# Kernel tuning notes

Measured on AMD Instinct MI355X. Metric: run time of the kernel, lower is better.

## Reference

```python
import jax, jax.numpy as jnp
import numpy as np

N, E, G = 100000, 3200000, 5000
EPS = 1e-5
HEADS, HC = 8, 16


def setup_inputs() -> dict:
    key = jax.random.key(0)
    k = jax.random.split(key, 12)

    def lin(kk, fi, fo):
        return (jax.random.normal(kk, (fi, fo), jnp.float32) / np.sqrt(fi)).astype(jnp.float32)

    return {
        "x": jax.random.normal(k[0], (N, 20), jnp.float32),
        "edge_index": jax.random.randint(k[1], (2, E), 0, N, dtype=jnp.int32),
        "batch": jnp.sort(jax.random.randint(k[2], (N,), 0, G, dtype=jnp.int32)),
        "W1": lin(k[3], 20, 64), "b1": jnp.zeros((64,), jnp.float32),
        "g1": jnp.ones((64,), jnp.float32), "be1": jnp.zeros((64,), jnp.float32),
        "W2": lin(k[4], 64, 32), "b2": jnp.zeros((32,), jnp.float32),
        "g2": jnp.ones((32,), jnp.float32), "be2": jnp.zeros((32,), jnp.float32),
        "W3": lin(k[5], 32, 16), "b3": jnp.zeros((16,), jnp.float32),
        "g3": jnp.ones((16,), jnp.float32), "be3": jnp.zeros((16,), jnp.float32),
        "Wg": lin(k[6], 16, HEADS * HC),
        "att_src": jax.random.normal(k[7], (HEADS, HC), jnp.float32) * 0.1,
        "att_dst": jax.random.normal(k[8], (HEADS, HC), jnp.float32) * 0.1,
        "bg": jnp.zeros((HC,), jnp.float32),
        "Wf": lin(k[9], 16, 3), "bf": jnp.zeros((3,), jnp.float32),
    }


def reference(x, edge_index, batch,
              W1, b1, g1, be1, W2, b2, g2, be2, W3, b3, g3, be3,
              Wg, att_src, att_dst, bg, Wf, bf):
    src, dst = edge_index[0], edge_index[1]
    loop = jnp.arange(N, dtype=src.dtype)
    src_sl = jnp.concatenate([src, loop])  # self-loops (GCN + GAT add_self_loops)
    dst_sl = jnp.concatenate([dst, loop])

    # GCN symmetric normalization D^-1/2 (A+I) D^-1/2
    deg = jax.ops.segment_sum(jnp.ones_like(src_sl, dtype=jnp.float32), dst_sl, N)
    dinv = jnp.where(deg > 0, 1.0 / jnp.sqrt(deg), 0.0)
    norm = (dinv[src_sl] * dinv[dst_sl])[:, None]  # [E+N, 1]

    def gcn(h, W, b):
        h = h @ W
        return jax.ops.segment_sum(h[src_sl] * norm, dst_sl, N) + b

    def bn_relu(h, g, b):  # BatchNorm1d (train-mode batch stats) + ReLU
        mu = h.mean(0)
        var = ((h - mu) ** 2).mean(0)
        return jax.nn.relu(g * (h - mu) * jax.lax.rsqrt(var + EPS) + b)

    h = bn_relu(gcn(x, W1, b1), g1, be1)   # dropout = identity (eval)
    h = bn_relu(gcn(h, W2, b2), g2, be2)
    h = bn_relu(gcn(h, W3, b3), g3, be3)

    # GATConv: heads=8, concat=False (mean over heads), eval -> no dropout
    xg = (h @ Wg).reshape(N, HEADS, HC)
    a_src = (xg * att_src).sum(-1)  # [N, H]
    a_dst = (xg * att_dst).sum(-1)
    logit = jax.nn.leaky_relu(a_src[src_sl] + a_dst[dst_sl], 0.2)  # [E+N, H]
    m = jax.ops.segment_max(logit, dst_sl, N)          # segment softmax over dst
    e = jnp.exp(logit - m[dst_sl])
    s = jax.ops.segment_sum(e, dst_sl, N)
    alpha = e / s[dst_sl]
    agg = jax.ops.segment_sum(xg[src_sl] * alpha[:, :, None], dst_sl, N)  # [N,H,C]
    hg = agg.mean(1) + bg  # [N, 16]

    pooled = jax.ops.segment_sum(hg, batch, G)  # global_add_pool -> [G, 16]
    return pooled @ Wf + bf  # [G, 3]
```

## Files before the change

kernel.cpp:

```cpp
#include <hip/hip_runtime.h>
#include <hip/hip_fp16.h>

constexpr int NN = 100000;
constexpr int EE = 3200000;
constexpr int GG = 5000;
constexpr float BNEPS = 1e-5f;

constexpr int BINS = 128;
constexpr int NPB = (NN + BINS - 1) / BINS;
constexpr int BCHUNK = 8192;
constexpr int NBCH = (EE + BCHUNK - 1) / BCHUNK;
constexpr int BINCAP2 = 96;
constexpr int BINREG = 27648;
constexpr int LCAP = 26624;
constexpr int CTR_STRIDE = 32;

typedef int int4v __attribute__((ext_vector_type(4)));


__global__ __launch_bounds__(1024) void bin_edges(const int* __restrict__ ei,
                                                  uint2* __restrict__ pairs,
                                                  int* __restrict__ binCur) {
    __shared__ int bcnt[BINS];
    __shared__ int bbase[BINS];
    __shared__ uint2 buf[BINS][BINCAP2];
    const int t = threadIdx.x;
    const int lane = t & 63, wv = t >> 6;
    for (int ch = blockIdx.x; ch < NBCH; ch += gridDim.x) {
        for (int k = t; k < BINS; k += 1024) bcnt[k] = 0;
        __syncthreads();
        const int qbase = ch * (BCHUNK / 4);
#pragma unroll
        for (int rep = 0; rep < 2; ++rep) {
            const int q = qbase + rep * 1024 + t;
            if (q < EE / 4) {
                int4v d = __builtin_nontemporal_load((const int4v*)(ei + EE) + q);
                int4v s = __builtin_nontemporal_load((const int4v*)ei + q);
                int dd[4] = {d.x, d.y, d.z, d.w};
                int ss[4] = {s.x, s.y, s.z, s.w};
#pragma unroll
                for (int k = 0; k < 4; ++k) {
                    int o = dd[k] / NPB;
                    int p = atomicAdd(&bcnt[o], 1);
                    if (p < BINCAP2) {
                        buf[o][p] = make_uint2((unsigned)dd[k], (unsigned)ss[k]);
                    } else {
                        int gp = atomicAdd(&binCur[o * CTR_STRIDE], 1);
                        pairs[(size_t)o * BINREG + gp] =
                            make_uint2((unsigned)dd[k], (unsigned)ss[k]);
                    }
                }
            }
        }
        __syncthreads();
        if (t < BINS) {
            int c = bcnt[t] < BINCAP2 ? bcnt[t] : BINCAP2;
            bbase[t] = atomicAdd(&binCur[t * CTR_STRIDE], c);
            bcnt[t] = c;
        }
        __syncthreads();
        for (int o = wv; o < BINS; o += 16) {
            const int c = bcnt[o];
            const size_t base = (size_t)o * BINREG + bbase[o];
            for (int k = lane; k < c; k += 64) pairs[base + k] = buf[o][k];
        }
        __syncthreads();
    }
}


__global__ void bin_base(const int* __restrict__ binCur, int* __restrict__ binBase) {
    __shared__ int s[BINS];
    const int t = threadIdx.x;
    const int v = binCur[t * CTR_STRIDE];
    s[t] = v;
    __syncthreads();
    for (int off = 1; off < BINS; off <<= 1) {
        int add = (t >= off) ? s[t - off] : 0;
        __syncthreads();
        s[t] += add;
        __syncthreads();
    }
    binBase[t] = s[t] - v;
}


__global__ __launch_bounds__(1024) void scatter_lds(const uint2* __restrict__ pairs,
                                                    const int* __restrict__ binCur,
                                                    const int* __restrict__ binBase,
                                                    int* __restrict__ rowptr,
                                                    float* __restrict__ dinv,
                                                    int* __restrict__ colA) {
    __shared__ int scnt[NPB];
    __shared__ int sscan[1024];
    __shared__ int lbuf[LCAP];
    const int b = blockIdx.x;
    const int t = threadIdx.x;
    const int lo = b * NPB;
    const int hi = (lo + NPB < NN) ? lo + NPB : NN;
    const int nb = hi - lo;
    const int tot = binCur[b * CTR_STRIDE];
    const int base = binBase[b];
    const uint2* p = pairs + (size_t)b * BINREG;
    for (int k = t; k < nb; k += 1024) scnt[k] = 0;
    __syncthreads();
    for (int q = t; q < tot; q += 1024) atomicAdd(&scnt[p[q].x - lo], 1);
    __syncthreads();
    const int myc = (t < nb) ? scnt[t] : 0;
    sscan[t] = myc;
    __syncthreads();
    for (int off = 1; off < 1024; off <<= 1) {
        int add = (t >= off) ? sscan[t - off] : 0;
        __syncthreads();
        sscan[t] += add;
        __syncthreads();
    }
    const int excl = sscan[t] - myc;
    if (t < nb) {
        rowptr[lo + t] = base + excl;
        dinv[lo + t] = rsqrtf((float)(myc + 1));
        scnt[t] = excl;
    }
    if (b == BINS - 1 && t == 0) rowptr[NN] = base + tot;
    __syncthreads();
    for (int q = t; q < tot; q += 1024) {
        uint2 e = p[q];
        int pos = atomicAdd(&scnt[e.x - lo], 1);
        if (pos < LCAP) lbuf[pos] = (int)e.y;
        else colA[base + pos] = (int)e.y;
    }
    __syncthreads();
    const int m = tot < LCAP ? tot : LCAP;
    for (int k = t; k < m; k += 1024) colA[base + k] = lbuf[k];
}


__global__ void scale_x(const float* __restrict__ x, const float* __restrict__ dinv,
                        __half* __restrict__ xsc) {
    int idx = blockIdx.x * blockDim.x + threadIdx.x;
    if (idx < NN * 20) {
        int n = idx / 20;
        xsc[idx] = __float2half(x[idx] * dinv[n]);
    }
}


template <int FIN, int FOUT, bool AFFINE, bool SCALED, bool STATS>
__global__ void gemm_k(const float* __restrict__ hin,
                       const float* __restrict__ sumsIn, const float* __restrict__ ssqIn,
                       const float* __restrict__ g, const float* __restrict__ be,
                       const float* __restrict__ W, const float* __restrict__ dinv,
                       const float* __restrict__ bias,
                       float* __restrict__ outF, __half* __restrict__ outH,
                       float* __restrict__ sumsOut, float* __restrict__ ssqOut) {
    constexpr int NB = 256 / FOUT;
    __shared__ float Wl[FIN * FOUT];
    __shared__ float rows[NB][FIN];
    __shared__ float aa[AFFINE ? FIN : 1], bb[AFFINE ? FIN : 1];
    const int t = threadIdx.x;
    if constexpr (AFFINE) {
        if (t < FIN) {
            float mu = sumsIn[t] / (float)NN;
            float var = ssqIn[t] / (float)NN - mu * mu;
            float a = g[t] * rsqrtf(var + BNEPS);
            aa[t] = a;
            bb[t] = be[t] - mu * a;
        }
    }
    for (int i = t; i < FIN * FOUT; i += 256) Wl[i] = W[i];
    const int c = t % FOUT, s = t / FOUT;
    const int ngrp = (NN + NB - 1) / NB;
    float sAcc = 0.f, qAcc = 0.f;
    for (int grp = blockIdx.x; grp < ngrp; grp += gridDim.x) {
        __syncthreads();
        for (int i = t; i < NB * FIN; i += 256) {
            int sn = i / FIN, k = i % FIN;
            int n2 = grp * NB + sn;
            float v = 0.f;
            if (n2 < NN) {
                v = hin[(size_t)n2 * FIN + k];
                if constexpr (AFFINE) {
                    v = aa[k] * v + bb[k];
                    v = v > 0.f ? v : 0.f;
                }
            }
            rows[sn][k] = v;
        }
        __syncthreads();
        int node = grp * NB + s;
        if (node < NN) {
            float acc = 0.f;
#pragma unroll
            for (int k = 0; k < FIN; ++k) acc += rows[s][k] * Wl[k * FOUT + c];
            if constexpr (SCALED) {
                outH[(size_t)node * FOUT + c] = __float2half(acc * dinv[node]);
            } else {
                float val = acc + bias[c];
                outF[(size_t)node * FOUT + c] = val;
                if constexpr (STATS) { sAcc += val; qAcc += val * val; }
            }
        }
    }
    if constexpr (STATS) {
        __shared__ float ls[FOUT], lq[FOUT];
        __syncthreads();
        if (t < FOUT) { ls[t] = 0.f; lq[t] = 0.f; }
        __syncthreads();
        atomicAdd(&ls[c], sAcc);
        atomicAdd(&lq[c], qAcc);
        __syncthreads();
        if (t < FOUT) { atomicAdd(&sumsOut[t], ls[t]); atomicAdd(&ssqOut[t], lq[t]); }
    }
}


template <int H2, int OUTF, bool STATS>
__global__ void agg_half(const __half2* __restrict__ src, const int* __restrict__ rowptr,
                         const int* __restrict__ colA, const float* __restrict__ dinv,
                         const float* __restrict__ bias, float* __restrict__ out,
                         float* __restrict__ sumsOut, float* __restrict__ ssqOut) {
    constexpr int SUB = 64 / H2;
    const int lane = threadIdx.x & 63;
    const int wid = (blockIdx.x * blockDim.x + threadIdx.x) >> 6;
    const int totalWaves = (gridDim.x * blockDim.x) >> 6;
    const int f = lane % H2;
    const int sub = lane / H2;
    const int stride = totalWaves * SUB;
    float bx = 0.f, by = 0.f;
    if (bias != nullptr) {
        bx = bias[2 * f];
        by = (2 * f + 1 < OUTF) ? bias[2 * f + 1] : 0.f;
    }
    const int i0 = (sub < SUB) ? wid * SUB + sub : NN;
    float sx = 0.f, qx = 0.f, sy = 0.f, qy = 0.f;
    for (int i = i0; i < NN; i += stride) {
        const int r0 = rowptr[i], r1 = rowptr[i + 1];
        float2 acc = __half22float2(src[(size_t)i * H2 + f]);
        float2 acc2 = {0.f, 0.f};
        int e = r0;
        for (; e + 3 < r1; e += 4) {
            int j0 = colA[e], j1 = colA[e + 1], j2 = colA[e + 2], j3 = colA[e + 3];
            float2 v0 = __half22float2(src[(size_t)j0 * H2 + f]);
            float2 v1 = __half22float2(src[(size_t)j1 * H2 + f]);
            float2 v2 = __half22float2(src[(size_t)j2 * H2 + f]);
            float2 v3 = __half22float2(src[(size_t)j3 * H2 + f]);
            acc.x += v0.x + v1.x;
            acc.y += v0.y + v1.y;
            acc2.x += v2.x + v3.x;
            acc2.y += v2.y + v3.y;
        }
        for (; e < r1; ++e) {
            float2 v = __half22float2(src[(size_t)colA[e] * H2 + f]);
            acc.x += v.x; acc.y += v.y;
        }
        acc.x += acc2.x; acc.y += acc2.y;
        const float d = dinv[i];
        float vx = d * acc.x + bx;
        out[(size_t)i * OUTF + 2 * f] = vx;
        if constexpr (STATS) { sx += vx; qx += vx * vx; }
        if (2 * f + 1 < OUTF) {
            float vy = d * acc.y + by;
            out[(size_t)i * OUTF + 2 * f + 1] = vy;
            if constexpr (STATS) { sy += vy; qy += vy * vy; }
        }
    }
    if constexpr (STATS) {
        __shared__ float ls[OUTF], lq[OUTF];
        const int t = threadIdx.x;
        if (t < OUTF) { ls[t] = 0.f; lq[t] = 0.f; }
        __syncthreads();
        atomicAdd(&ls[2 * f], sx);
        atomicAdd(&lq[2 * f], qx);
        if (2 * f + 1 < OUTF) {
            atomicAdd(&ls[2 * f + 1], sy);
            atomicAdd(&lq[2 * f + 1], qy);
        }
        __syncthreads();
        if (t < OUTF) { atomicAdd(&sumsOut[t], ls[t]); atomicAdd(&ssqOut[t], lq[t]); }
    }
}


__global__ void gat_mats(const float* __restrict__ Wg, const float* __restrict__ att_src,
                         const float* __restrict__ att_dst, const float* __restrict__ Wf,
                         const float* __restrict__ bg, float* __restrict__ Psrc,
                         float* __restrict__ Pdst, float* __restrict__ M,
                         float* __restrict__ bgW) {
    int t = threadIdx.x;
    if (t < 128) {
        int k = t >> 3, h = t & 7;
        float s = 0.f, d = 0.f;
        for (int c = 0; c < 16; ++c) {
            float wv = Wg[k * 128 + h * 16 + c];
            s += wv * att_src[h * 16 + c];
            d += wv * att_dst[h * 16 + c];
        }
        Psrc[k * 8 + h] = s;
        Pdst[k * 8 + h] = d;
    } else if (t < 512) {
        int m = t - 128;
        if (m < 384) {
            int hk = m / 3, j = m - hk * 3;
            int H = hk >> 4, k = hk & 15;
            float s = 0.f;
            for (int c = 0; c < 16; ++c) s += Wg[k * 128 + H * 16 + c] * Wf[c * 3 + j];
            M[hk * 3 + j] = 0.125f * s;
        }
    } else if (t < 515) {
        int j = t - 512;
        float s = 0.f;
        for (int c = 0; c < 16; ++c) s += bg[c] * Wf[c * 3 + j];
        bgW[j] = s;
    }
}


__global__ void gat_pre2(const float* __restrict__ h3,
                         const float* __restrict__ sums3, const float* __restrict__ ssq3,
                         const float* __restrict__ g3, const float* __restrict__ be3,
                         const float* __restrict__ Psrc, const float* __restrict__ Pdst,
                         __half* __restrict__ z, float* __restrict__ asrc,
                         float* __restrict__ adst) {
    __shared__ float Ps[128], Pd[128], aa[16], bb[16];
    int t = threadIdx.x;
    if (t < 128) { Ps[t] = Psrc[t]; Pd[t] = Pdst[t]; }
    if (t < 16) {
        float mu = sums3[t] / (float)NN;
        float var = ssq3[t] / (float)NN - mu * mu;
        float a = g3[t] * rsqrtf(var + BNEPS);
        aa[t] = a;
        bb[t] = be3[t] - mu * a;
    }
    __syncthreads();
    int n = blockIdx.x * blockDim.x + t;
    if (n >= NN) return;
    float zv[16];
#pragma unroll
    for (int k = 0; k < 16; ++k) {
        float v = h3[(size_t)n * 16 + k];
        v = aa[k] * v + bb[k];
        zv[k] = v > 0.f ? v : 0.f;
    }
    __half2 zh[8];
#pragma unroll
    for (int k = 0; k < 8; ++k) zh[k] = __floats2half2_rn(zv[2 * k], zv[2 * k + 1]);
    float4* zo = (float4*)(z + (size_t)n * 16);
    zo[0] = ((float4*)zh)[0];
    zo[1] = ((float4*)zh)[1];
    float as[8], ad[8];
#pragma unroll
    for (int h = 0; h < 8; ++h) { as[h] = 0.f; ad[h] = 0.f; }
#pragma unroll
    for (int k = 0; k < 16; ++k) {
        float zk = zv[k];
#pragma unroll
        for (int h = 0; h < 8; ++h) {
            as[h] += zk * Ps[k * 8 + h];
            ad[h] += zk * Pd[k * 8 + h];
        }
    }
    float4* a4 = (float4*)(asrc + (size_t)n * 8);
    a4[0] = make_float4(as[0], as[1], as[2], as[3]);
    a4[1] = make_float4(as[4], as[5], as[6], as[7]);
    float4* d4 = (float4*)(adst + (size_t)n * 8);
    d4[0] = make_float4(ad[0], ad[1], ad[2], ad[3]);
    d4[1] = make_float4(ad[4], ad[5], ad[6], ad[7]);
}


__device__ __forceinline__ float leaky02(float x) { return x > 0.f ? x : 0.2f * x; }

__global__ void gat_agg5(const float2* __restrict__ z2, const float* __restrict__ asrc,
                         const float* __restrict__ adst, const int* __restrict__ rowptr,
                         const int* __restrict__ colA, __half* __restrict__ Sn) {
    const int lane = threadIdx.x & 63;
    const int q = lane & 3;
    const int hh = (lane >> 2) & 1;
    const int sub = lane >> 3;
    const int wid = (blockIdx.x * blockDim.x + threadIdx.x) >> 6;
    const int totalWaves = (gridDim.x * blockDim.x) >> 6;
    const float4* asrc4 = (const float4*)asrc;
    const float4* adst4 = (const float4*)adst;
    for (int i = wid; i < NN; i += totalWaves) {
        const int r0 = rowptr[i], r1 = rowptr[i + 1];
        const float4 adh = adst4[(size_t)i * 2 + hh];
        float acc[4][4];
        float wsum[4];
        {
            float4 a = asrc4[(size_t)i * 2 + hh];
            float2 zr = z2[(size_t)i * 4 + q];
            const __half2* zp = (const __half2*)&zr;
            float2 f0 = __half22float2(zp[0]), f1 = __half22float2(zp[1]);
            float zf[4] = {f0.x, f0.y, f1.x, f1.y};
            float wq[4];
            wq[0] = (sub == 0) ? __expf(leaky02(a.x + adh.x)) : 0.f;
            wq[1] = (sub == 0) ? __expf(leaky02(a.y + adh.y)) : 0.f;
            wq[2] = (sub == 0) ? __expf(leaky02(a.z + adh.z)) : 0.f;
            wq[3] = (sub == 0) ? __expf(leaky02(a.w + adh.w)) : 0.f;
#pragma unroll
            for (int h = 0; h < 4; ++h) {
                wsum[h] = wq[h];
#pragma unroll
                for (int k = 0; k < 4; ++k) acc[h][k] = wq[h] * zf[k];
            }
        }
        for (int e = r0; e < r1; e += 8) {
            const int ee = e + sub;
            const bool val = ee < r1;
            const int j = val ? colA[ee] : i;
            float4 a = asrc4[(size_t)j * 2 + hh];
            float2 zr = z2[(size_t)j * 4 + q];
            const __half2* zp = (const __half2*)&zr;
            float2 f0 = __half22float2(zp[0]), f1 = __half22float2(zp[1]);
            float zf[4] = {f0.x, f0.y, f1.x, f1.y};
            float wq[4];
            wq[0] = val ? __expf(leaky02(a.x + adh.x)) : 0.f;
            wq[1] = val ? __expf(leaky02(a.y + adh.y)) : 0.f;
            wq[2] = val ? __expf(leaky02(a.z + adh.z)) : 0.f;
            wq[3] = val ? __expf(leaky02(a.w + adh.w)) : 0.f;
#pragma unroll
            for (int h = 0; h < 4; ++h) {
                wsum[h] += wq[h];
#pragma unroll
                for (int k = 0; k < 4; ++k) acc[h][k] += wq[h] * zf[k];
            }
        }
#pragma unroll
        for (int off = 8; off < 64; off <<= 1) {
#pragma unroll
            for (int h = 0; h < 4; ++h) {
                wsum[h] += __shfl_xor(wsum[h], off);
#pragma unroll
                for (int k = 0; k < 4; ++k) acc[h][k] += __shfl_xor(acc[h][k], off);
            }
        }
        if (lane < 8) {
#pragma unroll
            for (int h = 0; h < 4; ++h) {
                const float inv = 1.f / wsum[h];
                __half2 o[2];
                o[0] = __floats2half2_rn(acc[h][0] * inv, acc[h][1] * inv);
                o[1] = __floats2half2_rn(acc[h][2] * inv, acc[h][3] * inv);
                *(float2*)(Sn + (size_t)i * 128 + (hh * 4 + h) * 16 + q * 4) = *(float2*)o;
            }
        }
    }
}


__global__ void graph_bounds(const int* __restrict__ batch, int* __restrict__ gstart) {
    int n = blockIdx.x * blockDim.x + threadIdx.x;
    if (n < NN) {
        int bn = batch[n];
        int bp = (n == 0) ? -1 : batch[n - 1];
        for (int g = bp + 1; g <= bn; ++g) gstart[g] = n;
        if (n == NN - 1)
            for (int g = bn + 1; g <= GG; ++g) gstart[g] = NN;
    }
}


__global__ void pool_final(const __half2* __restrict__ Sn2, const int* __restrict__ gstart,
                           const float* __restrict__ M, const float* __restrict__ bgW,
                           const float* __restrict__ bf, float* __restrict__ out) {
    const int lane = threadIdx.x & 63;
    const int g = (blockIdx.x * blockDim.x + threadIdx.x) >> 6;
    if (g >= GG) return;
    const int n0 = gstart[g], n1 = gstart[g + 1];
    float2 s = {0.f, 0.f};
    for (int n = n0; n < n1; ++n) {
        float2 v = __half22float2(Sn2[(size_t)n * 64 + lane]);
        s.x += v.x;
        s.y += v.y;
    }
    float o[3];
#pragma unroll
    for (int j = 0; j < 3; ++j)
        o[j] = s.x * M[(2 * lane) * 3 + j] + s.y * M[(2 * lane + 1) * 3 + j];
#pragma unroll
    for (int off = 1; off < 64; off <<= 1) {
#pragma unroll
        for (int j = 0; j < 3; ++j) o[j] += __shfl_xor(o[j], off);
    }
    if (lane == 0) {
        float cnt = (float)(n1 - n0);
#pragma unroll
        for (int j = 0; j < 3; ++j) out[g * 3 + j] = o[j] + cnt * bgW[j] + bf[j];
    }
}


extern "C" void kernel_launch(void* const* d_in, const int* in_sizes, int n_in,
                              void* d_out, int out_size, void* d_ws, size_t ws_size,
                              hipStream_t stream) {
    const float* x = (const float*)d_in[0];
    const int* ei = (const int*)d_in[1];
    const int* batch = (const int*)d_in[2];
    const float* W1 = (const float*)d_in[3];  const float* b1 = (const float*)d_in[4];
    const float* g1 = (const float*)d_in[5];  const float* be1 = (const float*)d_in[6];
    const float* W2 = (const float*)d_in[7];  const float* b2 = (const float*)d_in[8];
    const float* g2 = (const float*)d_in[9];  const float* be2 = (const float*)d_in[10];
    const float* W3 = (const float*)d_in[11]; const float* b3 = (const float*)d_in[12];
    const float* g3 = (const float*)d_in[13]; const float* be3 = (const float*)d_in[14];
    const float* Wg = (const float*)d_in[15];
    const float* att_src = (const float*)d_in[16];
    const float* att_dst = (const float*)d_in[17];
    const float* bg = (const float*)d_in[18];
    const float* Wf = (const float*)d_in[19];
    const float* bf = (const float*)d_in[20];
    float* out = (float*)d_out;

    char* w = (char*)d_ws;
    auto alloc = [&](size_t bytes) -> char* {
        char* p = w;
        w += (bytes + 255) & ~(size_t)255;
        return p;
    };
    int* binCur = (int*)alloc((size_t)BINS * CTR_STRIDE * 4);
    float* sums1 = (float*)alloc(64 * 4); float* ssq1 = (float*)alloc(64 * 4);
    float* sums2 = (float*)alloc(32 * 4); float* ssq2 = (float*)alloc(32 * 4);
    float* sums3 = (float*)alloc(16 * 4); float* ssq3 = (float*)alloc(16 * 4);
    size_t zeroBytes = (size_t)(w - (char*)d_ws);
    int* binBase = (int*)alloc((size_t)BINS * 4);
    float* Psrc = (float*)alloc(128 * 4);
    float* Pdst = (float*)alloc(128 * 4);
    float* Mm = (float*)alloc(384 * 4);
    float* bgW = (float*)alloc(3 * 4);
    int* gstart = (int*)alloc((size_t)(GG + 1) * 4);
    int* rowptr = (int*)alloc((size_t)(NN + 1) * 4);
    int* colA = (int*)alloc((size_t)EE * 4);
    float* dinv = (float*)alloc((size_t)NN * 4);
    char* A = alloc((size_t)NN * 64 * 4);
    char* B = alloc((size_t)NN * 64 * 4);

    uint2*  pairs = (uint2*)A;
    __half* xsc  = (__half*)B;
    float*  aggx = (float*)(B + (size_t)NN * 32 * 2);
    float*  h1   = (float*)A;
    __half* hs2  = (__half*)B;
    float*  h2   = (float*)(B + (size_t)NN * 32 * 2);
    __half* hs3  = (__half*)A;
    float*  h3   = (float*)(A + (size_t)NN * 16 * 2);
    __half* z    = (__half*)(A + (size_t)NN * 24 * 4);
    float*  asrc = (float*)(A + (size_t)NN * 32 * 4);
    float*  adst = (float*)(A + (size_t)NN * 40 * 4);
    __half* Sn   = (__half*)B;

    hipMemsetAsync(d_ws, 0, zeroBytes, stream);

    bin_edges<<<256, 1024, 0, stream>>>(ei, pairs, binCur);
    bin_base<<<1, BINS, 0, stream>>>(binCur, binBase);
    scatter_lds<<<BINS, 1024, 0, stream>>>(pairs, binCur, binBase, rowptr, dinv, colA);
    gat_mats<<<1, 1024, 0, stream>>>(Wg, att_src, att_dst, Wf, bg, Psrc, Pdst, Mm, bgW);
    graph_bounds<<<(NN + 255) / 256, 256, 0, stream>>>(batch, gstart);

    scale_x<<<(NN * 20 + 255) / 256, 256, 0, stream>>>(x, dinv, xsc);
    agg_half<10, 20, false><<<2048, 256, 0, stream>>>((const __half2*)xsc, rowptr, colA, dinv,
                                                      nullptr, aggx, nullptr, nullptr);
    gemm_k<20, 64, false, false, true><<<2048, 256, 0, stream>>>(
        aggx, nullptr, nullptr, nullptr, nullptr, W1, dinv, b1, h1, nullptr, sums1, ssq1);

    gemm_k<64, 32, true, true, false><<<2048, 256, 0, stream>>>(
        h1, sums1, ssq1, g1, be1, W2, dinv, nullptr, nullptr, hs2, nullptr, nullptr);
    agg_half<16, 32, true><<<2048, 256, 0, stream>>>((const __half2*)hs2, rowptr, colA, dinv,
                                                     b2, h2, sums2, ssq2);

    gemm_k<32, 16, true, true, false><<<2048, 256, 0, stream>>>(
        h2, sums2, ssq2, g2, be2, W3, dinv, nullptr, nullptr, hs3, nullptr, nullptr);
    agg_half<8, 16, true><<<2048, 256, 0, stream>>>((const __half2*)hs3, rowptr, colA, dinv,
                                                    b3, h3, sums3, ssq3);

    gat_pre2<<<(NN + 255) / 256, 256, 0, stream>>>(h3, sums3, ssq3, g3, be3, Psrc, Pdst,
                                                   z, asrc, adst);
    gat_agg5<<<2048, 256, 0, stream>>>((const float2*)z, asrc, adst, rowptr, colA, Sn);
    pool_final<<<(GG * 64 + 255) / 256, 256, 0, stream>>>((const __half2*)Sn, gstart, Mm, bgW,
                                                          bf, out);
}
```

Before: 515.5 us.

## Interleave GAT features with source logits and assign one node per 8-lane group

gat_pre2 now writes each node's half-precision features and its source attention logits into one 64-byte row, so every neighbor gather reads a single cache line instead of two separate arrays. gat_agg6 maps one destination node to each 8-lane group rather than one per wave. Each lane computes one head's exp weight and shares it through shuffles, and the group walks the edges serially with no cross-lane reduction at the end. The grid grows to 3200 blocks. Nodes with very different degrees now share a wave, which may cause divergence, and per-edge exp work drops from four per lane to one.

```diff
diff --git a/kernel.cpp b/kernel.cpp
--- a/kernel.cpp
+++ b/kernel.cpp
@@ -319,8 +319,7 @@
                          const float* __restrict__ sums3, const float* __restrict__ ssq3,
                          const float* __restrict__ g3, const float* __restrict__ be3,
                          const float* __restrict__ Psrc, const float* __restrict__ Pdst,
-                         __half* __restrict__ z, float* __restrict__ asrc,
-                         float* __restrict__ adst) {
+                         float4* __restrict__ zas, float* __restrict__ adst) {
     __shared__ float Ps[128], Pd[128], aa[16], bb[16];
     int t = threadIdx.x;
     if (t < 128) { Ps[t] = Psrc[t]; Pd[t] = Pdst[t]; }
@@ -344,9 +343,6 @@
     __half2 zh[8];
 #pragma unroll
     for (int k = 0; k < 8; ++k) zh[k] = __floats2half2_rn(zv[2 * k], zv[2 * k + 1]);
-    float4* zo = (float4*)(z + (size_t)n * 16);
-    zo[0] = ((float4*)zh)[0];
-    zo[1] = ((float4*)zh)[1];
     float as[8], ad[8];
 #pragma unroll
     for (int h = 0; h < 8; ++h) { as[h] = 0.f; ad[h] = 0.f; }
@@ -359,9 +355,11 @@
             ad[h] += zk * Pd[k * 8 + h];
         }
     }
-    float4* a4 = (float4*)(asrc + (size_t)n * 8);
-    a4[0] = make_float4(as[0], as[1], as[2], as[3]);
-    a4[1] = make_float4(as[4], as[5], as[6], as[7]);
+    float4* zrow = zas + (size_t)n * 4;
+    zrow[0] = ((float4*)zh)[0];
+    zrow[1] = ((float4*)zh)[1];
+    zrow[2] = make_float4(as[0], as[1], as[2], as[3]);
+    zrow[3] = make_float4(as[4], as[5], as[6], as[7]);
     float4* d4 = (float4*)(adst + (size_t)n * 8);
     d4[0] = make_float4(ad[0], ad[1], ad[2], ad[3]);
     d4[1] = make_float4(ad[4], ad[5], ad[6], ad[7]);
@@ -370,79 +368,57 @@
 
 __device__ __forceinline__ float leaky02(float x) { return x > 0.f ? x : 0.2f * x; }
 
-__global__ void gat_agg5(const float2* __restrict__ z2, const float* __restrict__ asrc,
-                         const float* __restrict__ adst, const int* __restrict__ rowptr,
-                         const int* __restrict__ colA, __half* __restrict__ Sn) {
+__global__ void gat_agg6(const float4* __restrict__ zas, const float* __restrict__ adst,
+                         const int* __restrict__ rowptr, const int* __restrict__ colA,
+                         __half* __restrict__ Sn) {
     const int lane = threadIdx.x & 63;
-    const int q = lane & 3;
-    const int hh = (lane >> 2) & 1;
-    const int sub = lane >> 3;
+    const int ls = lane & 7;
+    const int q = ls & 3;
+    const int hh = ls >> 2;
+    const int grp = lane >> 3;
+    const int gb = lane & 56;
     const int wid = (blockIdx.x * blockDim.x + threadIdx.x) >> 6;
     const int totalWaves = (gridDim.x * blockDim.x) >> 6;
-    const float4* asrc4 = (const float4*)asrc;
-    const float4* adst4 = (const float4*)adst;
-    for (int i = wid; i < NN; i += totalWaves) {
+    const int stride = totalWaves * 8;
+    const char* zb = (const char*)zas;
+    for (int i = wid * 8 + grp; i < NN; i += stride) {
         const int r0 = rowptr[i], r1 = rowptr[i + 1];
-        const float4 adh = adst4[(size_t)i * 2 + hh];
+        const float adv = adst[(size_t)i * 8 + ls];
         float acc[4][4];
         float wsum[4];
-        {
-            float4 a = asrc4[(size_t)i * 2 + hh];
-            float2 zr = z2[(size_t)i * 4 + q];
+#pragma unroll
+        for (int h = 0; h < 4; ++h) {
+            wsum[h] = 0.f;
+#pragma unroll
+            for (int k = 0; k < 4; ++k) acc[h][k] = 0.f;
+        }
+        auto body = [&](int j) {
+            const char* row = zb + (size_t)j * 64;
+            const float av = *(const float*)(row + 32 + ls * 4);
+            const float2 zr = *(const float2*)(row + q * 8);
             const __half2* zp = (const __half2*)&zr;
-            float2 f0 = __half22float2(zp[0]), f1 = __half22float2(zp[1]);
-            float zf[4] = {f0.x, f0.y, f1.x, f1.y};
+            const float2 f0 = __half22float2(zp[0]), f1 = __half22float2(zp[1]);
+            const float zf[4] = {f0.x, f0.y, f1.x, f1.y};
+            const float w = __expf(leaky02(av + adv));
             float wq[4];
-            wq[0] = (sub == 0) ? __expf(leaky02(a.x + adh.x)) : 0.f;
-            wq[1] = (sub == 0) ? __expf(leaky02(a.y + adh.y)) : 0.f;
-            wq[2] = (sub == 0) ? __expf(leaky02(a.z + adh.z)) : 0.f;
-            wq[3] = (sub == 0) ? __expf(leaky02(a.w + adh.w)) : 0.f;
-#pragma unroll
-            for (int h = 0; h < 4; ++h) {
-                wsum[h] = wq[h];
-#pragma unroll
-                for (int k = 0; k < 4; ++k) acc[h][k] = wq[h] * zf[k];
-            }
-        }
-        for (int e = r0; e < r1; e += 8) {
-            const int ee = e + sub;
-            const bool val = ee < r1;
-            const int j = val ? colA[ee] : i;
-            float4 a = asrc4[(size_t)j * 2 + hh];
-            float2 zr = z2[(size_t)j * 4 + q];
-            const __half2* zp = (const __half2*)&zr;
-            float2 f0 = __half22float2(zp[0]), f1 = __half22float2(zp[1]);
-            float zf[4] = {f0.x, f0.y, f1.x, f1.y};
-            float wq[4];
-            wq[0] = val ? __expf(leaky02(a.x + adh.x)) : 0.f;
-            wq[1] = val ? __expf(leaky02(a.y + adh.y)) : 0.f;
-            wq[2] = val ? __expf(leaky02(a.z + adh.z)) : 0.f;
-            wq[3] = val ? __expf(leaky02(a.w + adh.w)) : 0.f;
+#pragma unroll
+            for (int h = 0; h < 4; ++h) wq[h] = __shfl(w, gb + hh * 4 + h);
 #pragma unroll
             for (int h = 0; h < 4; ++h) {
                 wsum[h] += wq[h];
 #pragma unroll
                 for (int k = 0; k < 4; ++k) acc[h][k] += wq[h] * zf[k];
             }
-        }
-#pragma unroll
-        for (int off = 8; off < 64; off <<= 1) {
-#pragma unroll
-            for (int h = 0; h < 4; ++h) {
-                wsum[h] += __shfl_xor(wsum[h], off);
-#pragma unroll
-                for (int k = 0; k < 4; ++k) acc[h][k] += __shfl_xor(acc[h][k], off);
-            }
-        }
-        if (lane < 8) {
-#pragma unroll
-            for (int h = 0; h < 4; ++h) {
-                const float inv = 1.f / wsum[h];
-                __half2 o[2];
-                o[0] = __floats2half2_rn(acc[h][0] * inv, acc[h][1] * inv);
-                o[1] = __floats2half2_rn(acc[h][2] * inv, acc[h][3] * inv);
-                *(float2*)(Sn + (size_t)i * 128 + (hh * 4 + h) * 16 + q * 4) = *(float2*)o;
-            }
+        };
+        body(i);
+        for (int e = r0; e < r1; ++e) body(colA[e]);
+#pragma unroll
+        for (int h = 0; h < 4; ++h) {
+            const float inv = 1.f / wsum[h];
+            __half2 o[2];
+            o[0] = __floats2half2_rn(acc[h][0] * inv, acc[h][1] * inv);
+            o[1] = __floats2half2_rn(acc[h][2] * inv, acc[h][3] * inv);
+            *(float2*)(Sn + (size_t)i * 128 + (hh * 4 + h) * 16 + q * 4) = *(float2*)o;
         }
     }
 }
@@ -541,9 +517,8 @@
     float*  h2   = (float*)(B + (size_t)NN * 32 * 2);
     __half* hs3  = (__half*)A;
     float*  h3   = (float*)(A + (size_t)NN * 16 * 2);
-    __half* z    = (__half*)(A + (size_t)NN * 24 * 4);
-    float*  asrc = (float*)(A + (size_t)NN * 32 * 4);
-    float*  adst = (float*)(A + (size_t)NN * 40 * 4);
+    char*   zas  = A + (size_t)NN * 96;
+    float*  adst = (float*)(A + (size_t)NN * 160);
     __half* Sn   = (__half*)B;
 
     hipMemsetAsync(d_ws, 0, zeroBytes, stream);
@@ -571,8 +546,8 @@
                                                     b3, h3, sums3, ssq3);
 
     gat_pre2<<<(NN + 255) / 256, 256, 0, stream>>>(h3, sums3, ssq3, g3, be3, Psrc, Pdst,
-                                                   z, asrc, adst);
-    gat_agg5<<<2048, 256, 0, stream>>>((const float2*)z, asrc, adst, rowptr, colA, Sn);
+                                                   (float4*)zas, adst);
+    gat_agg6<<<3200, 256, 0, stream>>>((const float4*)zas, adst, rowptr, colA, Sn);
     pool_final<<<(GG * 64 + 255) / 256, 256, 0, stream>>>((const __half2*)Sn, gstart, Mm, bgW,
                                                           bf, out);
 }
```

Measured after the change: 494.3 us. 4.1% less time.
